# Kernel optimization log

Measured on AMD Instinct MI355X. Metric: run time of the kernel, lower is better.

The kernel has to match this reference:

```python
import jax, jax.numpy as jnp
import numpy as np

BATCH, T, MAXLEN, DMODEL = 8, 32, 8, 256
UNITS = MAXLEN * DMODEL  # 2048, GRU units == input_dim


def setup_inputs() -> dict:
    key = jax.random.key(0)
    k1, k2, k3, k4, k5 = jax.random.split(key, 5)
    scale = 1.0 / np.sqrt(UNITS)
    x = jax.random.normal(k1, (BATCH, T, MAXLEN, DMODEL), jnp.float32)
    h0 = jax.random.normal(k2, (BATCH, UNITS), jnp.float32) * 0.1
    W = jax.random.normal(k3, (UNITS, 3 * UNITS), jnp.float32) * scale  # input kernel
    U = jax.random.normal(k4, (UNITS, 3 * UNITS), jnp.float32) * scale  # recurrent kernel
    b = jax.random.normal(k5, (2, 3 * UNITS), jnp.float32) * 0.01  # [input_bias, recurrent_bias] (reset_after)
    return {"x": x, "h0": h0, "W": W, "U": U, "b": b}


def _gru_seq(xp, h0, U, b_rec):
    """Run GRU (Keras v2, reset_after=True) over precomputed input projections.
    xp: (B, T, 3U) = x @ W + b_in ; h0: (B, U). Returns ((B,T,U) states, (B,U) last)."""
    def step(h, xp_t):
        rec = h @ U + b_rec  # (B, 3U)
        xz, xr, xh = jnp.split(xp_t, 3, axis=-1)
        rz, rr, rh = jnp.split(rec, 3, axis=-1)
        z = jax.nn.sigmoid(xz + rz)
        r = jax.nn.sigmoid(xr + rr)
        hh = jnp.tanh(xh + r * rh)
        h_new = z * h + (1.0 - z) * hh
        return h_new, h_new
    h_last, hs = jax.lax.scan(step, h0, jnp.swapaxes(xp, 0, 1))
    return jnp.swapaxes(hs, 0, 1), h_last


def reference(x, h0, W, U, b):
    # x: (B, T, M, d). Causal branch: for each mask row i, zero out positions > i
    # along the maxLen axis, run the full-sequence GRU, keep slice i of output.
    B, T, M, d = x.shape
    units = M * d
    b_in, b_rec = b[0], b[1]
    masks = jnp.tril(jnp.ones((M, M), x.dtype))  # (M, M) lower triangular
    # Fold the M mask variants into the batch dim -> one fused scan.
    xm = (x[None] * masks[:, None, None, :, None]).reshape(M * B, T, units)
    xp = jnp.einsum('bti,iu->btu', xm, W) + b_in  # precompute input projection
    h0r = jnp.broadcast_to(h0[None], (M, B, units)).reshape(M * B, units)
    hs, h_last = _gru_seq(xp, h0r, U, b_rec)
    out = hs.reshape(M, B, T, M, d)
    idx = jnp.arange(M)
    ret = out[idx, :, :, idx, :]            # (M, B, T, d): slice i of variant i
    ret = jnp.transpose(ret, (1, 2, 0, 3))  # (B, T, M, d)
    state = h_last.reshape(M, B, units)[M - 1]  # state from last (full-mask) run
    return ret, state
```

## Files before the change

### kernel.cpp

```cpp
#include <hip/hip_runtime.h>
#include <hip/hip_bf16.h>

typedef _Float16 f16x8 __attribute__((ext_vector_type(8)));
typedef float f32x4 __attribute__((ext_vector_type(4)));
typedef unsigned long long ull;

#define UNITS   2048
#define NC      6144
#define TSTEPS  32
#define HSTRIDE 131072

__device__ __forceinline__ float sigmoid_f(float v){ return 1.0f/(1.0f+__expf(-v)); }
__device__ __forceinline__ float tanh_f(float v){ return 2.0f/(1.0f+__expf(-2.0f*v)) - 1.0f; }

__global__ __launch_bounds__(256) void prep_misc(
    const float* __restrict__ x, const float* __restrict__ h0,
    _Float16* __restrict__ xh, _Float16* __restrict__ hRing,
    unsigned* __restrict__ bar)
{
  int i = blockIdx.x*256 + threadIdx.x;
  if (i < 640) bar[i] = 0;
  if (i < 524288) xh[i] = (_Float16)x[i];
  if (i < 131072) {
    int s = i >> 11, u = i & 2047;
    float v = h0[((s & 7) << 11) + u];
    hRing[(((u >> 3) << 6) + s)*8 + (u & 7)] = (_Float16)v;
  }
}

__global__ __launch_bounds__(256) void transpose_cast(
    const float* __restrict__ W, const float* __restrict__ U,
    _Float16* __restrict__ Wt, _Float16* __restrict__ Ut)
{
  __shared__ float tile[64][65];
  const float* src = blockIdx.z ? U : W;
  _Float16* dst = blockIdx.z ? Ut : Wt;
  int n0 = blockIdx.x*64, k0 = blockIdx.y*64;
  int lane = threadIdx.x & 63, grp = threadIdx.x >> 6;
  #pragma unroll
  for (int r = grp; r < 64; r += 4)
    tile[r][lane] = src[(size_t)(k0+r)*NC + n0 + lane];
  __syncthreads();
  #pragma unroll
  for (int r = grp; r < 64; r += 4)
    dst[(size_t)(n0+r)*UNITS + k0 + lane] = (_Float16)tile[lane][r];
}

__global__ __launch_bounds__(512) void xp_gemm(
    const _Float16* __restrict__ xh, const _Float16* __restrict__ Wt,
    const float* __restrict__ bin, _Float16* __restrict__ xpf)
{
  __shared__ __align__(16) short sB[64*256];
  int n0 = blockIdx.x*64, bt0 = blockIdx.y*128;
  int tid = threadIdx.x;
  int lane = tid & 63, w = tid >> 6;
  int wm = w & 3, wn = w >> 2;
  int nl = lane & 15, kg = lane >> 4;
  f32x4 acc[2][2] = {{{0,0,0,0},{0,0,0,0}},{{0,0,0,0},{0,0,0,0}}};
  for (int l = 0; l < 8; ++l) {
    __syncthreads();
    #pragma unroll
    for (int i = 0; i < 4; ++i) {
      int e = tid + i*512;
      int col = e >> 5, ch = e & 31;
      f16x8 v = *(const f16x8*)(Wt + (size_t)(n0+col)*UNITS + l*256 + ch*8);
      int off = ((col<<9) | (ch<<4)) ^ ((col&7)<<4);
      *(f16x8*)((char*)sB + off) = v;
    }
    __syncthreads();
    #pragma unroll
    for (int kk = 0; kk < 256; kk += 32) {
      f16x8 a[2];
      #pragma unroll
      for (int sub = 0; sub < 2; ++sub) {
        int row = bt0 + wm*32 + sub*16 + nl;
        a[sub] = *(const f16x8*)(xh + ((size_t)row*8 + l)*256 + kg*8 + kk);
      }
      #pragma unroll
      for (int nt = 0; nt < 2; ++nt) {
        int col = wn*32 + nt*16 + nl;
        int off = ((col<<9) | ((kk + kg*8)<<1)) ^ ((col&7)<<4);
        f16x8 bfr = *(const f16x8*)((const char*)sB + off);
        #pragma unroll
        for (int sub = 0; sub < 2; ++sub)
          acc[sub][nt] = __builtin_amdgcn_mfma_f32_16x16x32_f16(a[sub], bfr, acc[sub][nt], 0,0,0);
      }
    }
    #pragma unroll
    for (int sub = 0; sub < 2; ++sub) {
      int orow = bt0 + wm*32 + sub*16 + kg*4;
      #pragma unroll
      for (int nt = 0; nt < 2; ++nt) {
        int col = n0 + wn*32 + nt*16 + nl;
        float bv = bin[col];
        #pragma unroll
        for (int r = 0; r < 4; ++r) {
          int rr = orow + r;
          int b_ = rr >> 5, t_ = rr & 31;
          xpf[(size_t)((l*8 + b_)*32 + t_)*NC + col] = (_Float16)(acc[sub][nt][r] + bv);
        }
      }
    }
  }
}

__device__ __forceinline__ void half_barrier(unsigned* bar, int half, int idxInHalf, int t)
{
  __syncthreads();
  if (threadIdx.x == 0) {
    unsigned* grp  = bar + (half*8 + (idxInHalf & 7))*32;
    unsigned* root = bar + (16 + half)*32;
    unsigned tgt = (unsigned)(t + 1);
    unsigned a = __hip_atomic_fetch_add(grp, 1u, __ATOMIC_RELAXED, __HIP_MEMORY_SCOPE_AGENT) + 1u;
    if (a == tgt*16u)
      __hip_atomic_fetch_add(root, 1u, __ATOMIC_RELAXED, __HIP_MEMORY_SCOPE_AGENT);
    while (__hip_atomic_load(root, __ATOMIC_RELAXED, __HIP_MEMORY_SCOPE_AGENT) < tgt*8u)
      __builtin_amdgcn_s_sleep(1);
  }
  __syncthreads();
  __builtin_amdgcn_fence(__ATOMIC_ACQUIRE, "workgroup");
}

__global__ __launch_bounds__(512, 2) void gru_persist(
    const _Float16* __restrict__ Ut, const _Float16* __restrict__ xpf,
    const float* __restrict__ brec, const float* __restrict__ h0,
    _Float16* __restrict__ hRing,
    float* __restrict__ ret, float* __restrict__ st, unsigned* __restrict__ bar)
{
  __shared__ __align__(16) float sRed[48*288];

  int tid = threadIdx.x;
  int lane = tid & 63, kq = tid >> 6;
  int half = blockIdx.x & 1;
  int idxInHalf = blockIdx.x >> 1;
  int u0 = idxInHalf * 16;
  int s0 = half * 32;
  int nl = lane & 15, kg = lane >> 4;
  int redidx = lane*4 + (lane>>3)*4;

  f16x8 uw[3][8];
  #pragma unroll
  for (int g = 0; g < 3; ++g)
    #pragma unroll
    for (int kk = 0; kk < 8; ++kk) {
      uw[g][kk] = *(const f16x8*)(Ut + (size_t)(g*UNITS + u0 + nl)*UNITS + kq*256 + kk*32 + kg*8);
      asm volatile("" : "+v"(uw[g][kk]));
    }

  int s_local = tid >> 4, u_local = tid & 15;
  int sg = s0 + s_local;
  int u  = u0 + u_local;
  int mE = s_local >> 4, kgE = (s_local >> 2) & 3, rE = s_local & 3;
  int laneE = kgE*16 + u_local;
  int ridxE = laneE*4 + (laneE>>3)*4 + rE;
  int mm = u0 >> 8;

  float bz = brec[u], br = brec[2048+u], bh = brec[4096+u];
  float hprev = h0[((sg & 7) << 11) + u];

  for (int t = 0; t < TSTEPS; ++t) {
    const _Float16* hc = hRing + (size_t)t*HSTRIDE;
    _Float16*       hn = hRing + (size_t)(t+1)*HSTRIDE;

    const _Float16* xrow = xpf + ((size_t)sg*32 + t)*NC;
    float xz  = (float)xrow[u];
    float xr  = (float)xrow[2048+u];
    float xhv = (float)xrow[4096+u];

    f32x4 a0z={0,0,0,0}, a0r={0,0,0,0}, a0h={0,0,0,0};
    f32x4 a1z={0,0,0,0}, a1r={0,0,0,0}, a1h={0,0,0,0};
    const _Float16* Ab = hc + (size_t)(((kq*32 + kg)*64) + s0 + nl)*8;
    #pragma unroll
    for (int kk = 0; kk < 8; ++kk) {
      f16x8 av0 = *(const f16x8*)(Ab + kk*2048);
      f16x8 av1 = *(const f16x8*)(Ab + kk*2048 + 128);
      a0z = __builtin_amdgcn_mfma_f32_16x16x32_f16(av0, uw[0][kk], a0z, 0,0,0);
      a1z = __builtin_amdgcn_mfma_f32_16x16x32_f16(av1, uw[0][kk], a1z, 0,0,0);
      a0r = __builtin_amdgcn_mfma_f32_16x16x32_f16(av0, uw[1][kk], a0r, 0,0,0);
      a1r = __builtin_amdgcn_mfma_f32_16x16x32_f16(av1, uw[1][kk], a1r, 0,0,0);
      a0h = __builtin_amdgcn_mfma_f32_16x16x32_f16(av0, uw[2][kk], a0h, 0,0,0);
      a1h = __builtin_amdgcn_mfma_f32_16x16x32_f16(av1, uw[2][kk], a1h, 0,0,0);
    }

    {
      float* rp0 = &sRed[((kq*2 + 0)*3)*288 + redidx];
      *(f32x4*)(rp0)        = a0z;
      *(f32x4*)(rp0 + 288)  = a0r;
      *(f32x4*)(rp0 + 576)  = a0h;
      float* rp1 = &sRed[((kq*2 + 1)*3)*288 + redidx];
      *(f32x4*)(rp1)        = a1z;
      *(f32x4*)(rp1 + 288)  = a1r;
      *(f32x4*)(rp1 + 576)  = a1h;
    }
    __syncthreads();

    {
      float vz = 0.f, vr = 0.f, vh = 0.f;
      #pragma unroll
      for (int q = 0; q < 8; ++q) {
        const float* base = &sRed[((q*2 + mE)*3)*288 + ridxE];
        vz += base[0];
        vr += base[288];
        vh += base[576];
      }
      float z   = sigmoid_f(xz  + vz + bz);
      float rg  = sigmoid_f(xr  + vr + br);
      float hh  = tanh_f(xhv + rg*(vh + bh));
      float hnv = z*hprev + (1.0f - z)*hh;
      hprev = hnv;
      _Float16 hb = (_Float16)hnv;
      __hip_atomic_store((unsigned short*)hn + (size_t)(((u >> 3) << 6) + sg)*8 + (u & 7),
                         __builtin_bit_cast(unsigned short, hb),
                         __ATOMIC_RELAXED, __HIP_MEMORY_SCOPE_AGENT);
      if ((sg >> 3) == mm)
        ret[(size_t)((((sg & 7)*32 + t) << 3) + mm)*256 + (u & 255)] = hnv;
      if (t == 31 && sg >= 56)
        st[(size_t)(sg - 56)*UNITS + u] = hnv;
    }
    if (t < TSTEPS - 1)
      half_barrier(bar, half, idxInHalf, t);
  }
}

extern "C" void kernel_launch(void* const* d_in, const int* in_sizes, int n_in,
                              void* d_out, int out_size, void* d_ws, size_t ws_size,
                              hipStream_t stream) {
  const float* x  = (const float*)d_in[0];
  const float* h0 = (const float*)d_in[1];
  const float* W  = (const float*)d_in[2];
  const float* U  = (const float*)d_in[3];
  const float* b  = (const float*)d_in[4];
  float* ret = (float*)d_out;
  float* st  = ret + 524288;

  char* p = (char*)d_ws;
  _Float16* Ut = (_Float16*)p; p += 25165824;
  _Float16* Wt = (_Float16*)p; p += 25165824;
  _Float16* xh = (_Float16*)p; p += 1048576;
  _Float16* xpf = (_Float16*)p; p += 25165824;
  _Float16* hRing = (_Float16*)p; p += 33ull * HSTRIDE * 2;
  unsigned* bar = (unsigned*)p; p += 2560;

  prep_misc<<<2048, 256, 0, stream>>>(x, h0, xh, hRing, bar);
  transpose_cast<<<dim3(96,32,2), 256, 0, stream>>>(W, U, Wt, Ut);
  xp_gemm<<<dim3(96,2), 512, 0, stream>>>(xh, Wt, b, xpf);

  const float* brec = b + NC;
  void* args[] = { (void*)&Ut, (void*)&xpf, (void*)&brec, (void*)&h0,
                   (void*)&hRing, (void*)&ret, (void*)&st, (void*)&bar };
  hipLaunchCooperativeKernel((const void*)gru_persist, dim3(256), dim3(512),
                             args, 0, stream);
}
```

Baseline: 257.9 us.

## Fuse weight transpose and input projection GEMM into persistent GRU kernel

Removes the separate transpose_cast and xp_gemm kernels. Each persistent block now reads its own column slice of W and U directly from fp32, casts it to fp16 in shared memory, computes its slice of the input projection into a block-private buffer, and loads its recurrent weights from LDS. This avoids writing and re-reading the full fp16 transposed weights and the full projection tensor, and saves two launches. The cost is that the fp32 weight reads now use strided 16-byte chunks, and the projection GEMM runs on only 256 blocks before the recurrence starts.

```diff
diff --git a/kernel.cpp b/kernel.cpp
--- a/kernel.cpp
+++ b/kernel.cpp
@@ -9,6 +9,7 @@
 #define NC      6144
 #define TSTEPS  32
 #define HSTRIDE 131072
+#define XPB_STRIDE 98304
 
 __device__ __forceinline__ float sigmoid_f(float v){ return 1.0f/(1.0f+__expf(-v)); }
 __device__ __forceinline__ float tanh_f(float v){ return 2.0f/(1.0f+__expf(-2.0f*v)) - 1.0f; }
@@ -28,82 +29,6 @@
   }
 }
 
-__global__ __launch_bounds__(256) void transpose_cast(
-    const float* __restrict__ W, const float* __restrict__ U,
-    _Float16* __restrict__ Wt, _Float16* __restrict__ Ut)
-{
-  __shared__ float tile[64][65];
-  const float* src = blockIdx.z ? U : W;
-  _Float16* dst = blockIdx.z ? Ut : Wt;
-  int n0 = blockIdx.x*64, k0 = blockIdx.y*64;
-  int lane = threadIdx.x & 63, grp = threadIdx.x >> 6;
-  #pragma unroll
-  for (int r = grp; r < 64; r += 4)
-    tile[r][lane] = src[(size_t)(k0+r)*NC + n0 + lane];
-  __syncthreads();
-  #pragma unroll
-  for (int r = grp; r < 64; r += 4)
-    dst[(size_t)(n0+r)*UNITS + k0 + lane] = (_Float16)tile[lane][r];
-}
-
-__global__ __launch_bounds__(512) void xp_gemm(
-    const _Float16* __restrict__ xh, const _Float16* __restrict__ Wt,
-    const float* __restrict__ bin, _Float16* __restrict__ xpf)
-{
-  __shared__ __align__(16) short sB[64*256];
-  int n0 = blockIdx.x*64, bt0 = blockIdx.y*128;
-  int tid = threadIdx.x;
-  int lane = tid & 63, w = tid >> 6;
-  int wm = w & 3, wn = w >> 2;
-  int nl = lane & 15, kg = lane >> 4;
-  f32x4 acc[2][2] = {{{0,0,0,0},{0,0,0,0}},{{0,0,0,0},{0,0,0,0}}};
-  for (int l = 0; l < 8; ++l) {
-    __syncthreads();
-    #pragma unroll
-    for (int i = 0; i < 4; ++i) {
-      int e = tid + i*512;
-      int col = e >> 5, ch = e & 31;
-      f16x8 v = *(const f16x8*)(Wt + (size_t)(n0+col)*UNITS + l*256 + ch*8);
-      int off = ((col<<9) | (ch<<4)) ^ ((col&7)<<4);
-      *(f16x8*)((char*)sB + off) = v;
-    }
-    __syncthreads();
-    #pragma unroll
-    for (int kk = 0; kk < 256; kk += 32) {
-      f16x8 a[2];
-      #pragma unroll
-      for (int sub = 0; sub < 2; ++sub) {
-        int row = bt0 + wm*32 + sub*16 + nl;
-        a[sub] = *(const f16x8*)(xh + ((size_t)row*8 + l)*256 + kg*8 + kk);
-      }
-      #pragma unroll
-      for (int nt = 0; nt < 2; ++nt) {
-        int col = wn*32 + nt*16 + nl;
-        int off = ((col<<9) | ((kk + kg*8)<<1)) ^ ((col&7)<<4);
-        f16x8 bfr = *(const f16x8*)((const char*)sB + off);
-        #pragma unroll
-        for (int sub = 0; sub < 2; ++sub)
-          acc[sub][nt] = __builtin_amdgcn_mfma_f32_16x16x32_f16(a[sub], bfr, acc[sub][nt], 0,0,0);
-      }
-    }
-    #pragma unroll
-    for (int sub = 0; sub < 2; ++sub) {
-      int orow = bt0 + wm*32 + sub*16 + kg*4;
-      #pragma unroll
-      for (int nt = 0; nt < 2; ++nt) {
-        int col = n0 + wn*32 + nt*16 + nl;
-        float bv = bin[col];
-        #pragma unroll
-        for (int r = 0; r < 4; ++r) {
-          int rr = orow + r;
-          int b_ = rr >> 5, t_ = rr & 31;
-          xpf[(size_t)((l*8 + b_)*32 + t_)*NC + col] = (_Float16)(acc[sub][nt][r] + bv);
-        }
-      }
-    }
-  }
-}
-
 __device__ __forceinline__ void half_barrier(unsigned* bar, int half, int idxInHalf, int t)
 {
   __syncthreads();
@@ -121,16 +46,18 @@
   __builtin_amdgcn_fence(__ATOMIC_ACQUIRE, "workgroup");
 }
 
-__global__ __launch_bounds__(512, 2) void gru_persist(
-    const _Float16* __restrict__ Ut, const _Float16* __restrict__ xpf,
-    const float* __restrict__ brec, const float* __restrict__ h0,
-    _Float16* __restrict__ hRing,
+__global__ __launch_bounds__(512, 2) void gru_mega(
+    const float* __restrict__ W, const float* __restrict__ U,
+    const float* __restrict__ b, const float* __restrict__ h0,
+    const _Float16* __restrict__ xh,
+    _Float16* __restrict__ xpb, _Float16* __restrict__ hRing,
     float* __restrict__ ret, float* __restrict__ st, unsigned* __restrict__ bar)
 {
   __shared__ __align__(16) float sRed[48*288];
+  char* sStage = (char*)sRed;
 
   int tid = threadIdx.x;
-  int lane = tid & 63, kq = tid >> 6;
+  int lane = tid & 63, w8 = tid >> 6;
   int half = blockIdx.x & 1;
   int idxInHalf = blockIdx.x >> 1;
   int u0 = idxInHalf * 16;
@@ -138,15 +65,104 @@
   int nl = lane & 15, kg = lane >> 4;
   int redidx = lane*4 + (lane>>3)*4;
 
+  const float* bin  = b;
+  const float* brec = b + NC;
+  _Float16* myxp = xpb + (size_t)blockIdx.x * XPB_STRIDE;
+
+  {
+    float bv[3];
+    #pragma unroll
+    for (int g = 0; g < 3; ++g) bv[g] = bin[g*2048 + u0 + nl];
+    f32x4 acc[2][3];
+    #pragma unroll
+    for (int rt = 0; rt < 2; ++rt)
+      #pragma unroll
+      for (int ct = 0; ct < 3; ++ct) acc[rt][ct] = (f32x4){0,0,0,0};
+
+    for (int l = 0; l < 8; ++l) {
+      __syncthreads();
+      #pragma unroll
+      for (int i = 0; i < 6; ++i) {
+        int c = tid + i*512;
+        int k = c / 12, colq = c - k*12;
+        f32x4 v = *(const f32x4*)(W + (size_t)(l*256 + k)*NC
+                                    + (colq>>2)*2048 + u0 + (colq&3)*4);
+        #pragma unroll
+        for (int j = 0; j < 4; ++j) {
+          int cl = colq*4 + j;
+          int off = (cl*512 + k*2) ^ ((cl&7)<<4);
+          *(_Float16*)(sStage + off) = (_Float16)v[j];
+        }
+      }
+      __syncthreads();
+      #pragma unroll
+      for (int ks = 0; ks < 8; ++ks) {
+        f16x8 a[2];
+        #pragma unroll
+        for (int rt = 0; rt < 2; ++rt) {
+          int rbt = (w8*2 + rt)*16 + nl;
+          a[rt] = *(const f16x8*)(xh + ((size_t)rbt*8 + l)*256 + ks*32 + kg*8);
+        }
+        #pragma unroll
+        for (int ct = 0; ct < 3; ++ct) {
+          int cl = ct*16 + nl;
+          int off = (cl*512 + (ks*32 + kg*8)*2) ^ ((cl&7)<<4);
+          f16x8 bf = *(const f16x8*)(sStage + off);
+          #pragma unroll
+          for (int rt = 0; rt < 2; ++rt)
+            acc[rt][ct] = __builtin_amdgcn_mfma_f32_16x16x32_f16(a[rt], bf, acc[rt][ct], 0,0,0);
+        }
+      }
+      #pragma unroll
+      for (int rt = 0; rt < 2; ++rt)
+        #pragma unroll
+        for (int ct = 0; ct < 3; ++ct)
+          #pragma unroll
+          for (int r = 0; r < 4; ++r) {
+            int rbt = (w8*2 + rt)*16 + kg*4 + r;
+            int bb = rbt >> 5, tt = rbt & 31;
+            int s = l*8 + bb;
+            myxp[((size_t)(s*32 + tt)*3 + ct)*16 + nl] = (_Float16)(acc[rt][ct][r] + bv[ct]);
+          }
+    }
+  }
+
   f16x8 uw[3][8];
+  for (int band = 0; band < 8; ++band) {
+    __syncthreads();
+    #pragma unroll
+    for (int i = 0; i < 6; ++i) {
+      int c = tid + i*512;
+      int k = c / 12, colq = c - k*12;
+      f32x4 v = *(const f32x4*)(U + (size_t)(band*256 + k)*NC
+                                  + (colq>>2)*2048 + u0 + (colq&3)*4);
+      #pragma unroll
+      for (int j = 0; j < 4; ++j) {
+        int cl = colq*4 + j;
+        int off = (cl*512 + k*2) ^ ((cl&7)<<4);
+        *(_Float16*)(sStage + off) = (_Float16)v[j];
+      }
+    }
+    __syncthreads();
+    if (w8 == band) {
+      #pragma unroll
+      for (int g = 0; g < 3; ++g)
+        #pragma unroll
+        for (int kk = 0; kk < 8; ++kk) {
+          int cl = g*16 + nl;
+          int off = (cl*512 + (kk*32 + kg*8)*2) ^ ((cl&7)<<4);
+          uw[g][kk] = *(const f16x8*)(sStage + off);
+        }
+    }
+  }
   #pragma unroll
   for (int g = 0; g < 3; ++g)
     #pragma unroll
-    for (int kk = 0; kk < 8; ++kk) {
-      uw[g][kk] = *(const f16x8*)(Ut + (size_t)(g*UNITS + u0 + nl)*UNITS + kq*256 + kk*32 + kg*8);
+    for (int kk = 0; kk < 8; ++kk)
       asm volatile("" : "+v"(uw[g][kk]));
-    }
-
+  __syncthreads();
+
+  int kq = w8;
   int s_local = tid >> 4, u_local = tid & 15;
   int sg = s0 + s_local;
   int u  = u0 + u_local;
@@ -162,10 +178,10 @@
     const _Float16* hc = hRing + (size_t)t*HSTRIDE;
     _Float16*       hn = hRing + (size_t)(t+1)*HSTRIDE;
 
-    const _Float16* xrow = xpf + ((size_t)sg*32 + t)*NC;
-    float xz  = (float)xrow[u];
-    float xr  = (float)xrow[2048+u];
-    float xhv = (float)xrow[4096+u];
+    const _Float16* xrow = myxp + (size_t)(sg*32 + t)*48;
+    float xz  = (float)xrow[u_local];
+    float xr  = (float)xrow[16 + u_local];
+    float xhv = (float)xrow[32 + u_local];
 
     f32x4 a0z={0,0,0,0}, a0r={0,0,0,0}, a0h={0,0,0,0};
     f32x4 a1z={0,0,0,0}, a1r={0,0,0,0}, a1h={0,0,0,0};
@@ -234,20 +250,15 @@
   float* st  = ret + 524288;
 
   char* p = (char*)d_ws;
-  _Float16* Ut = (_Float16*)p; p += 25165824;
-  _Float16* Wt = (_Float16*)p; p += 25165824;
-  _Float16* xh = (_Float16*)p; p += 1048576;
-  _Float16* xpf = (_Float16*)p; p += 25165824;
+  _Float16* xh    = (_Float16*)p; p += 1048576;
+  _Float16* xpb   = (_Float16*)p; p += 256ull * XPB_STRIDE * 2;
   _Float16* hRing = (_Float16*)p; p += 33ull * HSTRIDE * 2;
-  unsigned* bar = (unsigned*)p; p += 2560;
+  unsigned* bar   = (unsigned*)p; p += 2560;
 
   prep_misc<<<2048, 256, 0, stream>>>(x, h0, xh, hRing, bar);
-  transpose_cast<<<dim3(96,32,2), 256, 0, stream>>>(W, U, Wt, Ut);
-  xp_gemm<<<dim3(96,2), 512, 0, stream>>>(xh, Wt, b, xpf);
-
-  const float* brec = b + NC;
-  void* args[] = { (void*)&Ut, (void*)&xpf, (void*)&brec, (void*)&h0,
-                   (void*)&hRing, (void*)&ret, (void*)&st, (void*)&bar };
-  hipLaunchCooperativeKernel((const void*)gru_persist, dim3(256), dim3(512),
+
+  void* args[] = { (void*)&W, (void*)&U, (void*)&b, (void*)&h0, (void*)&xh,
+                   (void*)&xpb, (void*)&hRing, (void*)&ret, (void*)&st, (void*)&bar };
+  hipLaunchCooperativeKernel((const void*)gru_mega, dim3(256), dim3(512),
                              args, 0, stream);
 }
```

Result: slower. 278.7 us (+8.1%).

## Fuse transpose-cast and input-projection GEMM into persistent cooperative GRU kernel

Applied to the files above, without the earlier changes.

Merges the weight transpose/cast kernel and the xp GEMM into the persistent cooperative GRU kernel as phases separated by grid-wide barriers. This removes two kernel launches and their gaps. The transpose also switches to vectorized float4 loads and f16x8 stores. In exchange, the transpose now runs on only 256 blocks instead of 6144 and the GEMM on 192 blocks, and the two grid barriers add overhead.

```diff
diff --git a/kernel.cpp b/kernel.cpp
--- a/kernel.cpp
+++ b/kernel.cpp
@@ -28,80 +28,21 @@
   }
 }
 
-__global__ __launch_bounds__(256) void transpose_cast(
-    const float* __restrict__ W, const float* __restrict__ U,
-    _Float16* __restrict__ Wt, _Float16* __restrict__ Ut)
-{
-  __shared__ float tile[64][65];
-  const float* src = blockIdx.z ? U : W;
-  _Float16* dst = blockIdx.z ? Ut : Wt;
-  int n0 = blockIdx.x*64, k0 = blockIdx.y*64;
-  int lane = threadIdx.x & 63, grp = threadIdx.x >> 6;
-  #pragma unroll
-  for (int r = grp; r < 64; r += 4)
-    tile[r][lane] = src[(size_t)(k0+r)*NC + n0 + lane];
-  __syncthreads();
-  #pragma unroll
-  for (int r = grp; r < 64; r += 4)
-    dst[(size_t)(n0+r)*UNITS + k0 + lane] = (_Float16)tile[lane][r];
-}
-
-__global__ __launch_bounds__(512) void xp_gemm(
-    const _Float16* __restrict__ xh, const _Float16* __restrict__ Wt,
-    const float* __restrict__ bin, _Float16* __restrict__ xpf)
-{
-  __shared__ __align__(16) short sB[64*256];
-  int n0 = blockIdx.x*64, bt0 = blockIdx.y*128;
-  int tid = threadIdx.x;
-  int lane = tid & 63, w = tid >> 6;
-  int wm = w & 3, wn = w >> 2;
-  int nl = lane & 15, kg = lane >> 4;
-  f32x4 acc[2][2] = {{{0,0,0,0},{0,0,0,0}},{{0,0,0,0},{0,0,0,0}}};
-  for (int l = 0; l < 8; ++l) {
-    __syncthreads();
-    #pragma unroll
-    for (int i = 0; i < 4; ++i) {
-      int e = tid + i*512;
-      int col = e >> 5, ch = e & 31;
-      f16x8 v = *(const f16x8*)(Wt + (size_t)(n0+col)*UNITS + l*256 + ch*8);
-      int off = ((col<<9) | (ch<<4)) ^ ((col&7)<<4);
-      *(f16x8*)((char*)sB + off) = v;
-    }
-    __syncthreads();
-    #pragma unroll
-    for (int kk = 0; kk < 256; kk += 32) {
-      f16x8 a[2];
-      #pragma unroll
-      for (int sub = 0; sub < 2; ++sub) {
-        int row = bt0 + wm*32 + sub*16 + nl;
-        a[sub] = *(const f16x8*)(xh + ((size_t)row*8 + l)*256 + kg*8 + kk);
-      }
-      #pragma unroll
-      for (int nt = 0; nt < 2; ++nt) {
-        int col = wn*32 + nt*16 + nl;
-        int off = ((col<<9) | ((kk + kg*8)<<1)) ^ ((col&7)<<4);
-        f16x8 bfr = *(const f16x8*)((const char*)sB + off);
-        #pragma unroll
-        for (int sub = 0; sub < 2; ++sub)
-          acc[sub][nt] = __builtin_amdgcn_mfma_f32_16x16x32_f16(a[sub], bfr, acc[sub][nt], 0,0,0);
-      }
-    }
-    #pragma unroll
-    for (int sub = 0; sub < 2; ++sub) {
-      int orow = bt0 + wm*32 + sub*16 + kg*4;
-      #pragma unroll
-      for (int nt = 0; nt < 2; ++nt) {
-        int col = n0 + wn*32 + nt*16 + nl;
-        float bv = bin[col];
-        #pragma unroll
-        for (int r = 0; r < 4; ++r) {
-          int rr = orow + r;
-          int b_ = rr >> 5, t_ = rr & 31;
-          xpf[(size_t)((l*8 + b_)*32 + t_)*NC + col] = (_Float16)(acc[sub][nt][r] + bv);
-        }
-      }
-    }
-  }
+__device__ __forceinline__ void phase_boundary(unsigned* ctr, unsigned nb)
+{
+  asm volatile("s_waitcnt vmcnt(0)" ::: "memory");
+  __syncthreads();
+  if (threadIdx.x == 0) {
+    __builtin_amdgcn_fence(__ATOMIC_RELEASE, "agent");
+    __hip_atomic_fetch_add(ctr, 1u, __ATOMIC_RELAXED, __HIP_MEMORY_SCOPE_AGENT);
+    while (__hip_atomic_load(ctr, __ATOMIC_RELAXED, __HIP_MEMORY_SCOPE_AGENT) < nb)
+      __builtin_amdgcn_s_sleep(1);
+    __builtin_amdgcn_fence(__ATOMIC_ACQUIRE, "agent");
+    __hip_atomic_fetch_add(ctr, 1u, __ATOMIC_RELAXED, __HIP_MEMORY_SCOPE_AGENT);
+    while (__hip_atomic_load(ctr, __ATOMIC_RELAXED, __HIP_MEMORY_SCOPE_AGENT) < 2u*nb)
+      __builtin_amdgcn_s_sleep(1);
+  }
+  __syncthreads();
 }
 
 __device__ __forceinline__ void half_barrier(unsigned* bar, int half, int idxInHalf, int t)
@@ -121,18 +62,108 @@
   __builtin_amdgcn_fence(__ATOMIC_ACQUIRE, "workgroup");
 }
 
-__global__ __launch_bounds__(512, 2) void gru_persist(
-    const _Float16* __restrict__ Ut, const _Float16* __restrict__ xpf,
-    const float* __restrict__ brec, const float* __restrict__ h0,
+__global__ __launch_bounds__(512, 2) void gru_all(
+    const float* __restrict__ W, const float* __restrict__ U,
+    const float* __restrict__ b, const float* __restrict__ h0,
+    const _Float16* __restrict__ xh,
+    _Float16* __restrict__ Wt, _Float16* __restrict__ Ut, _Float16* __restrict__ xpf,
     _Float16* __restrict__ hRing,
     float* __restrict__ ret, float* __restrict__ st, unsigned* __restrict__ bar)
 {
   __shared__ __align__(16) float sRed[48*288];
-
   int tid = threadIdx.x;
+  int bid = blockIdx.x;
+  unsigned nb = gridDim.x;
+
+  {
+    float (*tile)[65] = (float(*)[65])sRed;
+    for (int i = 0; i < 24; ++i) {
+      int lin = bid*24 + i;
+      int z = lin / 3072, rem = lin - z*3072;
+      int n0 = (rem % 96)*64, k0 = (rem / 96)*64;
+      const float* src = z ? U : W;
+      _Float16* dst = z ? Ut : Wt;
+      __syncthreads();
+      #pragma unroll
+      for (int p = 0; p < 2; ++p) {
+        int r = p*32 + (tid >> 4);
+        int nq = tid & 15;
+        f32x4 v = *(const f32x4*)(src + (size_t)(k0+r)*NC + n0 + nq*4);
+        tile[r][nq*4+0] = v[0];
+        tile[r][nq*4+1] = v[1];
+        tile[r][nq*4+2] = v[2];
+        tile[r][nq*4+3] = v[3];
+      }
+      __syncthreads();
+      {
+        int row = tid >> 3, k8 = (tid & 7)*8;
+        f16x8 o;
+        #pragma unroll
+        for (int j = 0; j < 8; ++j) o[j] = (_Float16)tile[k8+j][row];
+        *(f16x8*)(dst + (size_t)(n0+row)*UNITS + k0 + k8) = o;
+      }
+    }
+  }
+  phase_boundary(bar + 576, nb);
+
+  if (bid < 192) {
+    short* sB = (short*)sRed;
+    int n0 = (bid % 96)*64, bt0 = (bid / 96)*128;
+    int lane = tid & 63, w = tid >> 6;
+    int wm = w & 3, wn = w >> 2;
+    int nl = lane & 15, kg = lane >> 4;
+    f32x4 acc[2][2] = {{{0,0,0,0},{0,0,0,0}},{{0,0,0,0},{0,0,0,0}}};
+    for (int l = 0; l < 8; ++l) {
+      __syncthreads();
+      #pragma unroll
+      for (int i = 0; i < 4; ++i) {
+        int e = tid + i*512;
+        int col = e >> 5, ch = e & 31;
+        f16x8 v = *(const f16x8*)(Wt + (size_t)(n0+col)*UNITS + l*256 + ch*8);
+        int off = ((col<<9) | (ch<<4)) ^ ((col&7)<<4);
+        *(f16x8*)((char*)sB + off) = v;
+      }
+      __syncthreads();
+      #pragma unroll
+      for (int kk = 0; kk < 256; kk += 32) {
+        f16x8 a[2];
+        #pragma unroll
+        for (int sub = 0; sub < 2; ++sub) {
+          int row = bt0 + wm*32 + sub*16 + nl;
+          a[sub] = *(const f16x8*)(xh + ((size_t)row*8 + l)*256 + kg*8 + kk);
+        }
+        #pragma unroll
+        for (int nt = 0; nt < 2; ++nt) {
+          int col = wn*32 + nt*16 + nl;
+          int off = ((col<<9) | ((kk + kg*8)<<1)) ^ ((col&7)<<4);
+          f16x8 bfr = *(const f16x8*)((const char*)sB + off);
+          #pragma unroll
+          for (int sub = 0; sub < 2; ++sub)
+            acc[sub][nt] = __builtin_amdgcn_mfma_f32_16x16x32_f16(a[sub], bfr, acc[sub][nt], 0,0,0);
+        }
+      }
+      #pragma unroll
+      for (int sub = 0; sub < 2; ++sub) {
+        int orow = bt0 + wm*32 + sub*16 + kg*4;
+        #pragma unroll
+        for (int nt = 0; nt < 2; ++nt) {
+          int col = n0 + wn*32 + nt*16 + nl;
+          float bv = b[col];
+          #pragma unroll
+          for (int r = 0; r < 4; ++r) {
+            int rr = orow + r;
+            int b_ = rr >> 5, t_ = rr & 31;
+            xpf[(size_t)((l*8 + b_)*32 + t_)*NC + col] = (_Float16)(acc[sub][nt][r] + bv);
+          }
+        }
+      }
+    }
+  }
+  phase_boundary(bar + 608, nb);
+
   int lane = tid & 63, kq = tid >> 6;
-  int half = blockIdx.x & 1;
-  int idxInHalf = blockIdx.x >> 1;
+  int half = bid & 1;
+  int idxInHalf = bid >> 1;
   int u0 = idxInHalf * 16;
   int s0 = half * 32;
   int nl = lane & 15, kg = lane >> 4;
@@ -155,6 +186,7 @@
   int ridxE = laneE*4 + (laneE>>3)*4 + rE;
   int mm = u0 >> 8;
 
+  const float* brec = b + NC;
   float bz = brec[u], br = brec[2048+u], bh = brec[4096+u];
   float hprev = h0[((sg & 7) << 11) + u];
 
@@ -242,12 +274,10 @@
   unsigned* bar = (unsigned*)p; p += 2560;
 
   prep_misc<<<2048, 256, 0, stream>>>(x, h0, xh, hRing, bar);
-  transpose_cast<<<dim3(96,32,2), 256, 0, stream>>>(W, U, Wt, Ut);
-  xp_gemm<<<dim3(96,2), 512, 0, stream>>>(xh, Wt, b, xpf);
-
-  const float* brec = b + NC;
-  void* args[] = { (void*)&Ut, (void*)&xpf, (void*)&brec, (void*)&h0,
+
+  void* args[] = { (void*)&W, (void*)&U, (void*)&b, (void*)&h0, (void*)&xh,
+                   (void*)&Wt, (void*)&Ut, (void*)&xpf,
                    (void*)&hRing, (void*)&ret, (void*)&st, (void*)&bar };
-  hipLaunchCooperativeKernel((const void*)gru_persist, dim3(256), dim3(512),
+  hipLaunchCooperativeKernel((const void*)gru_all, dim3(256), dim3(512),
                              args, 0, stream);
 }
```

New measurement: 338.1 us. +31.1%, slower.
